# Kernel optimization log

Hardware: AMD Instinct MI355X
Metric: run time of the kernel (lower is better)

The kernel has to match this reference:

```python
import jax, jax.numpy as jnp
import numpy as np

N_SIGMA = 1
NUM_CLASS = 1
N_INST = 16          # max instance id (ids 1..16); instances==0 is background
W_INST, W_VAR, W_SEED = 1.0, 10.0, 1.0
H, W, B = 512, 512, 8
GRID = 1024          # buffer is linspace over 1024 then cropped to H,W


def make_xym(h, w, dtype=jnp.float32):
    full = jnp.linspace(0.0, 1.0, GRID, dtype=dtype)
    xm = jnp.broadcast_to(full[:w][None, :], (h, w))   # x varies along width
    ym = jnp.broadcast_to(full[:h][:, None], (h, w))   # y varies along height
    return jnp.stack([xm, ym], axis=0)                 # [2, H, W]


def lovasz_hinge_flat(logits, labels):
    # logits: [N] float, labels: [N] float in {0,1}
    signs = 2.0 * labels - 1.0
    errors = 1.0 - logits * signs
    order = jnp.argsort(-errors)
    errors_sorted = errors[order]
    gt_sorted = labels[order]
    gts = jnp.sum(gt_sorted)
    intersection = gts - jnp.cumsum(gt_sorted)
    union = gts + jnp.cumsum(1.0 - gt_sorted)
    jaccard = 1.0 - intersection / union
    grad = jnp.concatenate([jaccard[:1], jaccard[1:] - jaccard[:-1]])
    return jnp.sum(jax.nn.relu(errors_sorted) * grad)


def _per_image(pred, instance, label, xym):
    h, w = pred.shape[1], pred.shape[2]
    spatial_emb = jnp.tanh(pred[0:2]) + xym              # [2,H,W]
    sigma = pred[2:2 + N_SIGMA]                          # [n_sigma,H,W]
    seed = jax.nn.sigmoid(pred[2 + N_SIGMA])             # [H,W] (num_class==1)

    label_mask = (label == 1)
    bg_mask = (label == 0)
    seed_loss = jnp.sum(jnp.where(bg_mask, seed ** 2, 0.0))

    ids = jnp.arange(1, N_INST + 1)
    masks = (instance[None] == ids[:, None, None]) & label_mask[None]  # [K,H,W] bool
    maskf = masks.astype(pred.dtype)
    counts = jnp.sum(maskf, axis=(1, 2))                 # [K]
    present = counts > 0
    safe = jnp.maximum(counts, 1.0)

    # to_center=True: center = mean of xym coords over each instance mask
    center = jnp.einsum('khw,chw->kc', maskf, xym) / safe[:, None]        # [K,2]
    s_mean = jnp.einsum('khw,shw->ks', maskf, sigma) / safe[:, None]      # [K,n_sigma]

    # var loss: mean over in-mask pixels of (sigma - detached mean)^2
    dev2 = (sigma[None] - jax.lax.stop_gradient(s_mean)[:, :, None, None]) ** 2  # [K,ns,H,W]
    var_terms = jnp.einsum('khw,kshw->k', maskf, dev2) / (safe * N_SIGMA)

    # dist = exp(-s * sum_c (emb_c - center_c)^2), s = exp(10 * mean sigma)
    s_exp = jnp.exp(10.0 * s_mean)[:, 0]                 # [K] (n_sigma==1 broadcasts)
    diff2 = jnp.sum((spatial_emb[None] - center[:, :, None, None]) ** 2, axis=1)  # [K,H,W]
    dist = jnp.exp(-s_exp[:, None, None] * diff2)        # [K,H,W]

    inst_losses = jax.vmap(
        lambda d, m: lovasz_hinge_flat(2.0 * d.ravel() - 1.0, m.ravel())
    )(dist, maskf)
    instance_loss = jnp.sum(jnp.where(present, inst_losses, 0.0))
    var_loss = jnp.sum(jnp.where(present, var_terms, 0.0))

    seed_loss = seed_loss + jnp.sum(
        maskf * (seed[None] - jax.lax.stop_gradient(dist)) ** 2)

    obj = jnp.maximum(jnp.sum(present.astype(pred.dtype)), 1.0)
    return (W_INST * instance_loss / obj
            + W_VAR * var_loss / obj
            + W_SEED * seed_loss / (h * w))


def setup_inputs() -> dict:
    key = jax.random.key(0)
    k1, k2, k3 = jax.random.split(key, 3)
    prediction = jax.random.normal(k1, (B, 2 + N_SIGMA + NUM_CLASS, H, W), dtype=jnp.float32)
    instances = jax.random.randint(k2, (B, H, W), 0, N_INST + 1).astype(jnp.int64)
    labels = jax.random.randint(k3, (B, H, W), 0, NUM_CLASS + 1).astype(jnp.int64)
    return {"prediction": prediction, "instances": instances, "labels": labels}


def reference(prediction, instances, labels):
    xym = make_xym(prediction.shape[2], prediction.shape[3], prediction.dtype)
    per_img = jax.vmap(_per_image, in_axes=(0, 0, 0, None))(
        prediction, instances, labels, xym)
    return jnp.mean(per_img)
```

## Files before the change

kernel.cpp:

```cpp
#include <hip/hip_runtime.h>
#include <hip/hip_fp16.h>
#include <math.h>

#define HWPX 262144
#define NIMG 8
#define ACC_STRIDE 96
#define NB 1024
#define NSPLIT 32
#define NGRP 2

template<bool PACK>
__global__ __launch_bounds__(256) void k_prep(const float* __restrict__ pred,
    const int* __restrict__ inst, const int* __restrict__ lab,
    float2* __restrict__ exy, unsigned* __restrict__ meta, double* __restrict__ accd)
{
  __shared__ float s[81];
  int t = threadIdx.x;
  if (t < 81) s[t] = 0.0f;
  __syncthreads();
  int bid = blockIdx.x;
  int b = bid >> 7;
  int base = (bid & 127) << 11;
  const float* pb = pred + (size_t)b * 4 * HWPX;
  size_t ib = (size_t)b * HWPX;
  float bg = 0.0f;
  #pragma unroll
  for (int i = 0; i < 8; ++i) {
    int px = base + (i << 8) + t;
    int h = px >> 9, w = px & 511;
    float xm = w * (1.0f/1023.0f), ym = h * (1.0f/1023.0f);
    float sg = pb[2*HWPX + px];
    float p3 = pb[3*HWPX + px];
    float sd = 1.0f / (1.0f + __expf(-p3));
    int lv = lab[ib+px], iv = inst[ib+px];
    int mid = (lv == 1 && (unsigned)(iv-1) < 16u) ? iv : 0;
    if (PACK) {
      float ex = tanhf(pb[px]) + xm;
      float ey = tanhf(pb[HWPX+px]) + ym;
      exy[ib+px] = make_float2(ex, ey);
      unsigned hs = (unsigned)__half_as_ushort(__float2half(sd));
      meta[ib+px] = (hs << 16) | (unsigned)mid;
    }
    if (lv == 0) {
      bg += sd*sd;
    } else if (mid) {
      int k = mid - 1;
      atomicAdd(&s[k], 1.0f);
      atomicAdd(&s[16+k], xm);
      atomicAdd(&s[32+k], ym);
      atomicAdd(&s[48+k], sg);
      atomicAdd(&s[64+k], sg*sg);
    }
  }
  #pragma unroll
  for (int o = 32; o > 0; o >>= 1) bg += __shfl_down(bg, o);
  if ((t & 63) == 0) atomicAdd(&s[80], bg);
  __syncthreads();
  if (t < 81 && s[t] != 0.0f)
    atomicAdd(&accd[(size_t)b*ACC_STRIDE + t], (double)s[t]);
}

__global__ __launch_bounds__(128) void k_fin(double* __restrict__ accd, float* __restrict__ pairinfo)
{
  __shared__ double varr[128];
  __shared__ float pres[128];
  int t = threadIdx.x;
  int b = t >> 4, k = t & 15;
  double* ab = accd + (size_t)b*ACC_STRIDE;
  double cnt = ab[k];
  double safe = cnt > 0.0 ? cnt : 1.0;
  double ss = ab[48+k];
  double cx = ab[16+k]/safe, cy = ab[32+k]/safe, sm = ss/safe;
  double var = (ab[64+k] - ss*ss/safe)/safe;
  if (var < 0.0) var = 0.0;
  float4 pi = make_float4((float)cx, (float)cy, (float)exp(10.0*sm), (float)cnt);
  reinterpret_cast<float4*>(pairinfo)[t] = pi;
  pres[t] = cnt > 0.0 ? 1.0f : 0.0f;
  varr[t] = cnt > 0.0 ? var : 0.0;
  __syncthreads();
  if (t < NIMG) {
    float np = 0.0f; double vs = 0.0;
    for (int i = 0; i < 16; ++i) { np += pres[t*16+i]; vs += varr[t*16+i]; }
    double* ab2 = accd + (size_t)t*ACC_STRIDE;
    ab2[83] = vs;
    ab2[84] = (np > 1.0f) ? (double)np : 1.0;
  }
}

__global__ __launch_bounds__(1024) void k_hist(const float2* __restrict__ exy,
    const unsigned* __restrict__ meta, const float* __restrict__ pairinfo,
    unsigned* __restrict__ partial, double* __restrict__ accd)
{
  __shared__ unsigned hist[8*NB];
  __shared__ float redf[16];
  int t = threadIdx.x, bid = blockIdx.x;
  int b = bid & 7;
  int r = bid >> 3;
  int g = r & 1;
  int s = r >> 1;
  for (int i = t; i < 8*NB; i += 1024) hist[i] = 0u;
  float4 pi[8];
  #pragma unroll
  for (int j = 0; j < 8; ++j)
    pi[j] = reinterpret_cast<const float4*>(pairinfo)[b*16 + g*8 + j];
  __syncthreads();
  size_t base = (size_t)b*HWPX + (size_t)s*(HWPX/NSPLIT);
  float fit = 0.0f;
  for (int it = 0; it < HWPX/NSPLIT/1024; ++it) {
    size_t px = base + it*1024 + t;
    float2 e2 = exy[px];
    unsigned mv = meta[px];
    int mid = (int)(mv & 0xffu);
    float sd = __half2float(__ushort_as_half((unsigned short)(mv >> 16)));
    #pragma unroll
    for (int j = 0; j < 8; ++j) {
      float dx = e2.x - pi[j].x, dy = e2.y - pi[j].y;
      float d = __expf(-pi[j].z * (dx*dx + dy*dy));
      bool m = (mid == g*8 + j + 1);
      float e = m ? fmaf(-2.0f, d, 2.0f) : 2.0f*d;
      int key = (int)(e * (float)(NB/2));
      if (key > NB-1) key = NB-1;
      atomicAdd(&hist[j*NB + key], m ? 0x10000u : 1u);
      if (m) { float df = sd - d; fit += df*df; }
    }
  }
  #pragma unroll
  for (int o = 32; o > 0; o >>= 1) fit += __shfl_down(fit, o);
  if ((t & 63) == 0) redf[t >> 6] = fit;
  __syncthreads();
  if (t == 0) {
    float ft = 0.0f;
    for (int i = 0; i < 16; ++i) ft += redf[i];
    atomicAdd(&accd[(size_t)b*ACC_STRIDE + 81], (double)ft);
  }
  unsigned* pp = partial + (size_t)((b*NGRP + g)*NSPLIT + s)*(8*NB);
  for (int i = t; i < 8*NB; i += 1024) pp[i] = hist[i];
}

__global__ __launch_bounds__(1024) void k_scan(const unsigned* __restrict__ partial,
    const float* __restrict__ pairinfo, double* __restrict__ accd)
{
  __shared__ unsigned sp[NB], sq[NB];
  __shared__ float red[16];
  int t = threadIdx.x, bid = blockIdx.x;
  int b = bid >> 4, k = bid & 15;
  int g = k >> 3, j8 = k & 7;
  float G = pairinfo[(b*16 + k)*4 + 3];
  if (G <= 0.0f) return;
  unsigned p = 0, q = 0;
  const unsigned* basep = partial + (size_t)((b*NGRP + g)*NSPLIT)*(8*NB) + j8*NB + t;
  #pragma unroll 4
  for (int s2 = 0; s2 < NSPLIT; ++s2) {
    unsigned h = basep[(size_t)s2*(8*NB)];
    p += h >> 16; q += h & 0xffffu;
  }
  int j = (NB-1) - t;
  sp[j] = p; sq[j] = q;
  __syncthreads();
  for (int off = 1; off < NB; off <<= 1) {
    unsigned vp = 0, vq = 0;
    if (j >= off) { vp = sp[j-off]; vq = sq[j-off]; }
    __syncthreads();
    sp[j] += vp; sq[j] += vq;
    __syncthreads();
  }
  float A  = (float)(sp[j] - p);
  float Bn = (float)(sq[j] - q);
  float val = (t + 0.5f) * (2.0f/NB);
  float pf = (float)p, qf = (float)q;
  float Jb = (A + Bn) / (G + Bn);
  float Ja = (A + Bn + pf + qf) / (G + Bn + qf);
  float contrib = val * (Ja - Jb);
  #pragma unroll
  for (int o = 32; o > 0; o >>= 1) contrib += __shfl_down(contrib, o);
  if ((t & 63) == 0) red[t >> 6] = contrib;
  __syncthreads();
  if (t == 0) {
    float tot = 0.0f;
    for (int i = 0; i < 16; ++i) tot += red[i];
    atomicAdd(&accd[(size_t)b*ACC_STRIDE + 82], (double)tot);
  }
}

__global__ __launch_bounds__(1024) void k_lov_old(const float* __restrict__ pred,
    const int* __restrict__ inst, const int* __restrict__ lab,
    const float* __restrict__ pairinfo, double* __restrict__ accd)
{
  constexpr int SHIFT = 18;
  constexpr int NBB = (0x40000000 >> SHIFT) + 1;
  extern __shared__ unsigned char smem[];
  unsigned* histP = reinterpret_cast<unsigned*>(smem);
  unsigned* histQ = histP + NBB;
  unsigned* scanP = histQ + NBB;
  unsigned* scanQ = scanP + 1024;
  float* red  = reinterpret_cast<float*>(scanQ + 1024);
  float* redf = red + 16;
  int t = threadIdx.x, bid = blockIdx.x;
  int b = bid >> 4, k = bid & 15;
  float4 pi = reinterpret_cast<const float4*>(pairinfo)[bid];
  float cx = pi.x, cy = pi.y, sexp = pi.z, G = pi.w;
  if (G <= 0.0f) return;
  for (int i = t; i < 2*NBB; i += 1024) histP[i] = 0u;
  __syncthreads();
  size_t ib = (size_t)b * HWPX;
  const float* pb = pred + (size_t)b * 4 * HWPX;
  const int target = k + 1;
  float fit = 0.0f;
  for (int j = 0; j < HWPX/1024; ++j) {
    int px = (j << 10) + t;
    int h = px >> 9, w = px & 511;
    float ex = tanhf(pb[px]) + w*(1.0f/1023.0f);
    float ey = tanhf(pb[HWPX+px]) + h*(1.0f/1023.0f);
    float sd = 1.0f/(1.0f + __expf(-pb[3*HWPX+px]));
    int lv = lab[ib+px], iv = inst[ib+px];
    float dx = ex - cx, dy = ey - cy;
    float d = __expf(-sexp * (dx*dx + dy*dy));
    bool m = (lv == 1) && (iv == target);
    float e = m ? fmaf(-2.0f, d, 2.0f) : 2.0f * d;
    unsigned key = __float_as_uint(e) >> SHIFT;
    atomicAdd(m ? &histP[key] : &histQ[key], 1u);
    if (m) { float df = sd - d; fit += df*df; }
  }
  #pragma unroll
  for (int o = 32; o > 0; o >>= 1) fit += __shfl_down(fit, o);
  if ((t & 63) == 0) redf[t >> 6] = fit;
  __syncthreads();
  constexpr int CB = NBB / 1024;
  int start = (NBB - 1) - t * CB;
  int nk = (t == 1023) ? (CB + 1) : CB;
  unsigned lp = 0, lq = 0;
  for (int i = 0; i < nk; ++i) { lp += histP[start-i]; lq += histQ[start-i]; }
  scanP[t] = lp; scanQ[t] = lq;
  __syncthreads();
  for (int off = 1; off < 1024; off <<= 1) {
    unsigned vp = 0, vq = 0;
    if (t >= off) { vp = scanP[t-off]; vq = scanQ[t-off]; }
    __syncthreads();
    scanP[t] += vp; scanQ[t] += vq;
    __syncthreads();
  }
  float A  = (float)(scanP[t] - lp);
  float Bn = (float)(scanQ[t] - lq);
  float contrib = 0.0f;
  for (int i = 0; i < nk; ++i) {
    int kk = start - i;
    unsigned p = histP[kk], q = histQ[kk];
    if (p | q) {
      float lo = __uint_as_float((unsigned)kk << SHIFT);
      float hi = __uint_as_float((unsigned)(kk+1) << SHIFT);
      float valv = 0.5f*(lo+hi);
      if (valv > 2.0f) valv = 2.0f;
      float pq = (float)(p + q), qf = (float)q;
      float Jb = (A + Bn) / (G + Bn);
      float Ja = (A + Bn + pq) / (G + Bn + qf);
      contrib += valv * (Ja - Jb);
      A += (float)p; Bn += qf;
    }
  }
  #pragma unroll
  for (int o = 32; o > 0; o >>= 1) contrib += __shfl_down(contrib, o);
  if ((t & 63) == 0) red[t >> 6] = contrib;
  __syncthreads();
  if (t == 0) {
    float tot = 0.0f, ft = 0.0f;
    for (int i = 0; i < 16; ++i) { tot += red[i]; ft += redf[i]; }
    atomicAdd(&accd[(size_t)b*ACC_STRIDE + 82], (double)tot);
    atomicAdd(&accd[(size_t)b*ACC_STRIDE + 81], (double)ft);
  }
}

__global__ void k_final(const double* __restrict__ accd, float* __restrict__ out)
{
  int t = threadIdx.x;
  double lb = 0.0;
  if (t < NIMG) {
    const double* ab = accd + (size_t)t*ACC_STRIDE;
    lb = (ab[82] + 10.0*ab[83]) / ab[84] + (ab[80] + ab[81]) * (1.0/(double)HWPX);
  }
  #pragma unroll
  for (int o = 4; o > 0; o >>= 1) lb += __shfl_down(lb, o);
  if (t == 0) out[0] = (float)(lb * 0.125);
}

extern "C" void kernel_launch(void* const* d_in, const int* in_sizes, int n_in,
                              void* d_out, int out_size, void* d_ws, size_t ws_size,
                              hipStream_t stream)
{
  const float* pred = (const float*)d_in[0];
  const int*   inst = (const int*)d_in[1];
  const int*   lab  = (const int*)d_in[2];
  float* out = (float*)d_out;

  size_t exyB  = (size_t)NIMG * HWPX * sizeof(float2);
  size_t metaB = (size_t)NIMG * HWPX * sizeof(unsigned);
  size_t partB = (size_t)NIMG * NGRP * NSPLIT * 8 * NB * 4;
  size_t accB  = (size_t)NIMG * ACC_STRIDE * sizeof(double);
  size_t pairB = 128 * 4 * sizeof(float);
  bool full = ws_size >= exyB + metaB + partB + accB + pairB;

  char* ws = (char*)d_ws;
  if (full) {
    float2*   exy   = (float2*)ws;
    unsigned* meta  = (unsigned*)(ws + exyB);
    unsigned* part  = (unsigned*)(ws + exyB + metaB);
    double*   accd  = (double*)(ws + exyB + metaB + partB);
    float*    pairinfo = (float*)(ws + exyB + metaB + partB + accB);
    hipMemsetAsync(accd, 0, accB, stream);
    k_prep<true><<<1024,256,0,stream>>>(pred, inst, lab, exy, meta, accd);
    k_fin<<<1,128,0,stream>>>(accd, pairinfo);
    k_hist<<<NIMG*NGRP*NSPLIT,1024,0,stream>>>(exy, meta, pairinfo, part, accd);
    k_scan<<<128,1024,0,stream>>>(part, pairinfo, accd);
    k_final<<<1,64,0,stream>>>(accd, out);
  } else {
    double* accd = (double*)ws;
    float* pairinfo = (float*)(accd + NIMG*ACC_STRIDE);
    hipMemsetAsync(accd, 0, accB, stream);
    k_prep<false><<<1024,256,0,stream>>>(pred, inst, lab, nullptr, nullptr, accd);
    k_fin<<<1,128,0,stream>>>(accd, pairinfo);
    size_t lds18 = ((size_t)2*4097 + 2048)*4 + 128;
    k_lov_old<<<128,1024,lds18,stream>>>(pred, inst, lab, pairinfo, accd);
    k_final<<<1,64,0,stream>>>(accd, out);
  }
}
```

Baseline: 73.74 us.

## Pack per-pixel record into fp16 u64, bin negatives by distance, privatize prep atomics

The packed pixel data shrinks from a float2 plus a uint to one 64-bit record holding half-precision embedding x/y, seed and instance id. This cuts memory traffic in the histogram pass. Negative pixels skip the exp: they are binned by scaled squared distance up to ZMAX. The scan kernel then remaps those distance bins to error bins by evaluating exp at each bin centre. The prep kernel spreads its shared-memory atomics over 8 replicas to reduce contention. Risks are fp16 precision loss in the embeddings and a coarser binning error for negatives, including clipping at ZMAX.

```diff
diff --git a/kernel.cpp b/kernel.cpp
--- a/kernel.cpp
+++ b/kernel.cpp
@@ -6,23 +6,27 @@
 #define NIMG 8
 #define ACC_STRIDE 96
 #define NB 1024
+#define ZMAX 8.0f
 #define NSPLIT 32
 #define NGRP 2
+
+typedef unsigned long long u64;
 
 template<bool PACK>
 __global__ __launch_bounds__(256) void k_prep(const float* __restrict__ pred,
     const int* __restrict__ inst, const int* __restrict__ lab,
-    float2* __restrict__ exy, unsigned* __restrict__ meta, double* __restrict__ accd)
-{
-  __shared__ float s[81];
+    u64* __restrict__ rec, double* __restrict__ accd)
+{
+  __shared__ float s[8][83];
   int t = threadIdx.x;
-  if (t < 81) s[t] = 0.0f;
+  for (int i = t; i < 8*83; i += 256) (&s[0][0])[i] = 0.0f;
   __syncthreads();
   int bid = blockIdx.x;
   int b = bid >> 7;
   int base = (bid & 127) << 11;
   const float* pb = pred + (size_t)b * 4 * HWPX;
   size_t ib = (size_t)b * HWPX;
+  int r = t & 7;
   float bg = 0.0f;
   #pragma unroll
   for (int i = 0; i < 8; ++i) {
@@ -37,27 +41,33 @@
     if (PACK) {
       float ex = tanhf(pb[px]) + xm;
       float ey = tanhf(pb[HWPX+px]) + ym;
-      exy[ib+px] = make_float2(ex, ey);
-      unsigned hs = (unsigned)__half_as_ushort(__float2half(sd));
-      meta[ib+px] = (hs << 16) | (unsigned)mid;
+      u64 v = (u64)__half_as_ushort(__float2half(ex))
+            | ((u64)__half_as_ushort(__float2half(ey)) << 16)
+            | ((u64)__half_as_ushort(__float2half(sd)) << 32)
+            | ((u64)mid << 48);
+      rec[ib+px] = v;
     }
     if (lv == 0) {
       bg += sd*sd;
     } else if (mid) {
       int k = mid - 1;
-      atomicAdd(&s[k], 1.0f);
-      atomicAdd(&s[16+k], xm);
-      atomicAdd(&s[32+k], ym);
-      atomicAdd(&s[48+k], sg);
-      atomicAdd(&s[64+k], sg*sg);
+      atomicAdd(&s[r][k], 1.0f);
+      atomicAdd(&s[r][16+k], xm);
+      atomicAdd(&s[r][32+k], ym);
+      atomicAdd(&s[r][48+k], sg);
+      atomicAdd(&s[r][64+k], sg*sg);
     }
   }
   #pragma unroll
   for (int o = 32; o > 0; o >>= 1) bg += __shfl_down(bg, o);
-  if ((t & 63) == 0) atomicAdd(&s[80], bg);
-  __syncthreads();
-  if (t < 81 && s[t] != 0.0f)
-    atomicAdd(&accd[(size_t)b*ACC_STRIDE + t], (double)s[t]);
+  if ((t & 63) == 0) atomicAdd(&s[0][80], bg);
+  __syncthreads();
+  if (t < 81) {
+    float v = 0.0f;
+    #pragma unroll
+    for (int rr = 0; rr < 8; ++rr) v += s[rr][t];
+    if (v != 0.0f) atomicAdd(&accd[(size_t)b*ACC_STRIDE + t], (double)v);
+  }
 }
 
 __global__ __launch_bounds__(128) void k_fin(double* __restrict__ accd, float* __restrict__ pairinfo)
@@ -87,8 +97,8 @@
   }
 }
 
-__global__ __launch_bounds__(1024) void k_hist(const float2* __restrict__ exy,
-    const unsigned* __restrict__ meta, const float* __restrict__ pairinfo,
+__global__ __launch_bounds__(1024) void k_hist(const u64* __restrict__ rec,
+    const float* __restrict__ pairinfo,
     unsigned* __restrict__ partial, double* __restrict__ accd)
 {
   __shared__ unsigned hist[8*NB];
@@ -99,29 +109,39 @@
   int g = r & 1;
   int s = r >> 1;
   for (int i = t; i < 8*NB; i += 1024) hist[i] = 0u;
-  float4 pi[8];
-  #pragma unroll
-  for (int j = 0; j < 8; ++j)
-    pi[j] = reinterpret_cast<const float4*>(pairinfo)[b*16 + g*8 + j];
+  float cx[8], cy[8], se[8], s128[8];
+  #pragma unroll
+  for (int j = 0; j < 8; ++j) {
+    float4 pi = reinterpret_cast<const float4*>(pairinfo)[b*16 + g*8 + j];
+    cx[j] = pi.x; cy[j] = pi.y; se[j] = pi.z; s128[j] = pi.z * (float)(NB/ZMAX);
+  }
   __syncthreads();
   size_t base = (size_t)b*HWPX + (size_t)s*(HWPX/NSPLIT);
   float fit = 0.0f;
   for (int it = 0; it < HWPX/NSPLIT/1024; ++it) {
     size_t px = base + it*1024 + t;
-    float2 e2 = exy[px];
-    unsigned mv = meta[px];
-    int mid = (int)(mv & 0xffu);
-    float sd = __half2float(__ushort_as_half((unsigned short)(mv >> 16)));
+    u64 v = rec[px];
+    float ex = __half2float(__ushort_as_half((unsigned short)(v & 0xffffu)));
+    float ey = __half2float(__ushort_as_half((unsigned short)((v >> 16) & 0xffffu)));
+    float sd = __half2float(__ushort_as_half((unsigned short)((v >> 32) & 0xffffu)));
+    int rel = (int)(v >> 48) - 1 - g*8;
     #pragma unroll
     for (int j = 0; j < 8; ++j) {
-      float dx = e2.x - pi[j].x, dy = e2.y - pi[j].y;
-      float d = __expf(-pi[j].z * (dx*dx + dy*dy));
-      bool m = (mid == g*8 + j + 1);
-      float e = m ? fmaf(-2.0f, d, 2.0f) : 2.0f*d;
-      int key = (int)(e * (float)(NB/2));
-      if (key > NB-1) key = NB-1;
-      atomicAdd(&hist[j*NB + key], m ? 0x10000u : 1u);
-      if (m) { float df = sd - d; fit += df*df; }
+      float dx = ex - cx[j], dy = ey - cy[j];
+      float d2 = fmaf(dx, dx, dy*dy);
+      int key; unsigned add;
+      if (rel == j) {
+        float d = __expf(-d2 * se[j]);
+        float e = fmaf(-2.0f, d, 2.0f);
+        int kk = (int)(e * (float)(NB/2));
+        key = kk > NB-1 ? NB-1 : kk;
+        add = 0x10000u;
+        float df = sd - d; fit += df*df;
+      } else {
+        key = (int)fminf(d2 * s128[j], (float)(NB-1));
+        add = 1u;
+      }
+      atomicAdd(&hist[j*NB + key], add);
     }
   }
   #pragma unroll
@@ -147,6 +167,8 @@
   int g = k >> 3, j8 = k & 7;
   float G = pairinfo[(b*16 + k)*4 + 3];
   if (G <= 0.0f) return;
+  sq[t] = 0u;
+  __syncthreads();
   unsigned p = 0, q = 0;
   const unsigned* basep = partial + (size_t)((b*NGRP + g)*NSPLIT)*(8*NB) + j8*NB + t;
   #pragma unroll 4
@@ -154,8 +176,16 @@
     unsigned h = basep[(size_t)s2*(8*NB)];
     p += h >> 16; q += h & 0xffffu;
   }
+  float zmid = (t + 0.5f) * (ZMAX/NB);
+  float ev = 2.0f * __expf(-zmid);
+  int eb = (int)(ev * (float)(NB/2));
+  if (eb > NB-1) eb = NB-1;
+  if (q) atomicAdd(&sq[eb], q);
+  __syncthreads();
+  unsigned qe = sq[t];
+  __syncthreads();
   int j = (NB-1) - t;
-  sp[j] = p; sq[j] = q;
+  sp[j] = p; sq[j] = qe;
   __syncthreads();
   for (int off = 1; off < NB; off <<= 1) {
     unsigned vp = 0, vq = 0;
@@ -165,9 +195,9 @@
     __syncthreads();
   }
   float A  = (float)(sp[j] - p);
-  float Bn = (float)(sq[j] - q);
+  float Bn = (float)(sq[j] - qe);
   float val = (t + 0.5f) * (2.0f/NB);
-  float pf = (float)p, qf = (float)q;
+  float pf = (float)p, qf = (float)qe;
   float Jb = (A + Bn) / (G + Bn);
   float Ja = (A + Bn + pf + qf) / (G + Bn + qf);
   float contrib = val * (Ja - Jb);
@@ -291,31 +321,29 @@
   const int*   lab  = (const int*)d_in[2];
   float* out = (float*)d_out;
 
-  size_t exyB  = (size_t)NIMG * HWPX * sizeof(float2);
-  size_t metaB = (size_t)NIMG * HWPX * sizeof(unsigned);
+  size_t recB  = (size_t)NIMG * HWPX * sizeof(u64);
   size_t partB = (size_t)NIMG * NGRP * NSPLIT * 8 * NB * 4;
   size_t accB  = (size_t)NIMG * ACC_STRIDE * sizeof(double);
   size_t pairB = 128 * 4 * sizeof(float);
-  bool full = ws_size >= exyB + metaB + partB + accB + pairB;
+  bool full = ws_size >= recB + partB + accB + pairB;
 
   char* ws = (char*)d_ws;
   if (full) {
-    float2*   exy   = (float2*)ws;
-    unsigned* meta  = (unsigned*)(ws + exyB);
-    unsigned* part  = (unsigned*)(ws + exyB + metaB);
-    double*   accd  = (double*)(ws + exyB + metaB + partB);
-    float*    pairinfo = (float*)(ws + exyB + metaB + partB + accB);
+    u64*      rec   = (u64*)ws;
+    unsigned* part  = (unsigned*)(ws + recB);
+    double*   accd  = (double*)(ws + recB + partB);
+    float*    pairinfo = (float*)(ws + recB + partB + accB);
     hipMemsetAsync(accd, 0, accB, stream);
-    k_prep<true><<<1024,256,0,stream>>>(pred, inst, lab, exy, meta, accd);
+    k_prep<true><<<1024,256,0,stream>>>(pred, inst, lab, rec, accd);
     k_fin<<<1,128,0,stream>>>(accd, pairinfo);
-    k_hist<<<NIMG*NGRP*NSPLIT,1024,0,stream>>>(exy, meta, pairinfo, part, accd);
+    k_hist<<<NIMG*NGRP*NSPLIT,1024,0,stream>>>(rec, pairinfo, part, accd);
     k_scan<<<128,1024,0,stream>>>(part, pairinfo, accd);
     k_final<<<1,64,0,stream>>>(accd, out);
   } else {
     double* accd = (double*)ws;
     float* pairinfo = (float*)(accd + NIMG*ACC_STRIDE);
     hipMemsetAsync(accd, 0, accB, stream);
-    k_prep<false><<<1024,256,0,stream>>>(pred, inst, lab, nullptr, nullptr, accd);
+    k_prep<false><<<1024,256,0,stream>>>(pred, inst, lab, nullptr, accd);
     k_fin<<<1,128,0,stream>>>(accd, pairinfo);
     size_t lds18 = ((size_t)2*4097 + 2048)*4 + 128;
     k_lov_old<<<128,1024,lds18,stream>>>(pred, inst, lab, pairinfo, accd);
```

Result: no change. 72.84 us (-1.2%).
